# Kernel optimization log

Hardware: AMD Instinct MI355X
Metric: run time of the kernel (lower is better)

The kernel has to match this reference:

```python
import jax, jax.numpy as jnp
import numpy as np


def setup_inputs() -> dict:
    key = jax.random.key(0)
    k1, k2 = jax.random.split(key)
    B, T, S, D = 8, 1024, 1024, 2048
    support_sets = jax.random.normal(k1, (B, S, D), dtype=jnp.float32)
    X_hats = jax.random.normal(k2, (B, T, D), dtype=jnp.float32)
    return {"support_sets": support_sets, "X_hats": X_hats}


def reference(support_sets, X_hats):
    # Pairwise cosine similarity: out[b, t, s] = cos(X_hats[b, t], support_sets[b, s])
    # Matches torch.nn.functional.cosine_similarity with eps=1e-10:
    #   dot / max(||x|| * ||y||, eps)
    eps = 1e-10
    x_norm = jnp.linalg.norm(X_hats, axis=-1)          # [B, T]
    s_norm = jnp.linalg.norm(support_sets, axis=-1)    # [B, S]
    dots = jnp.einsum('btd,bsd->bts', X_hats, support_sets)  # [B, T, S]
    denom = jnp.maximum(x_norm[:, :, None] * s_norm[:, None, :], eps)
    return dots / denom
```

## Files before the change

kernel.cpp:

```cpp
#include <hip/hip_runtime.h>
#include <hip/hip_bf16.h>

typedef __attribute__((ext_vector_type(4))) float        f32x4;
typedef __attribute__((ext_vector_type(8))) short        s16x8;
typedef __attribute__((ext_vector_type(4))) unsigned int u32x4;
typedef __attribute__((ext_vector_type(2))) unsigned int u32x2;

#define Bb 8
#define Tt 1024
#define Ss 1024
#define Dd 2048
#define BM 128
#define BN 128
#define BK 64

__device__ __forceinline__ unsigned pack2_bf16(float f0, float f1) {
  unsigned u0 = __builtin_bit_cast(unsigned, f0) + 0x8000u;
  unsigned u1 = __builtin_bit_cast(unsigned, f1) + 0x8000u;
  return (u0 >> 16) | (u1 & 0xffff0000u);
}

__device__ __forceinline__ void gld_lds16(const void* g, void* l) {
  __builtin_amdgcn_global_load_lds(
      (__attribute__((address_space(1))) void*)(void*)(g),
      (__attribute__((address_space(3))) void*)l, 16, 0, 0);
}

__global__ __launch_bounds__(256, 8)
void convert_kernel(const float* __restrict__ src, unsigned* __restrict__ dst,
                    float* __restrict__ inv)
{
  __shared__ float red[4];
  const int row = blockIdx.x;
  const int t = threadIdx.x;
  const f32x4* s = (const f32x4*)(src + (size_t)row * Dd);
  const f32x4 a = s[t];
  const f32x4 b = s[256 + t];

  float sq = fmaf(a[0], a[0], fmaf(a[1], a[1], fmaf(a[2], a[2], a[3] * a[3])));
  sq = fmaf(b[0], b[0], fmaf(b[1], b[1], fmaf(b[2], b[2], fmaf(b[3], b[3], sq))));

  u32x2* d = (u32x2*)(dst + (size_t)row * (Dd / 2));
  d[t]       = (u32x2){pack2_bf16(a[0], a[1]), pack2_bf16(a[2], a[3])};
  d[256 + t] = (u32x2){pack2_bf16(b[0], b[1]), pack2_bf16(b[2], b[3])};

  #pragma unroll
  for (int m = 32; m; m >>= 1) sq += __shfl_xor(sq, m, 64);
  const int wave = t >> 6, lane = t & 63;
  if (lane == 0) red[wave] = sq;
  __syncthreads();
  if (t == 0) inv[row] = 1.0f / sqrtf(red[0] + red[1] + red[2] + red[3]);
}

__global__ __launch_bounds__(256, 2)
void gemm_kernel(const short* __restrict__ abf, const short* __restrict__ bbf,
                 const float* __restrict__ invA, const float* __restrict__ invB,
                 float* __restrict__ out)
{
  __shared__ short As[2][BM * BK];
  __shared__ short Bs[2][BN * BK];

  const int bid0 = blockIdx.x;
  const int bid  = ((bid0 & 7) << 6) | (bid0 >> 3);
  const int b    = bid >> 6;
  const int tile = bid & 63;
  const int tm   = tile >> 3;
  const int tn   = tile & 7;

  const int t = threadIdx.x, wave = t >> 6, lane = t & 63;

  const int srow = lane >> 3;
  const int cph  = lane & 7;
  const int r0   = wave * 32;

  const size_t aRow = (size_t)(b * Tt + tm * BM);
  const size_t bRow = (size_t)(b * Ss + tn * BN);
  const short *gA0, *gA1, *gA2, *gA3, *gB0, *gB1, *gB2, *gB3;
  {
    int r;
    r = r0 + 0 * 8 + srow; gA0 = abf + (aRow + r) * Dd + (cph ^ (r & 7)) * 8;
                           gB0 = bbf + (bRow + r) * Dd + (cph ^ (r & 7)) * 8;
    r = r0 + 1 * 8 + srow; gA1 = abf + (aRow + r) * Dd + (cph ^ (r & 7)) * 8;
                           gB1 = bbf + (bRow + r) * Dd + (cph ^ (r & 7)) * 8;
    r = r0 + 2 * 8 + srow; gA2 = abf + (aRow + r) * Dd + (cph ^ (r & 7)) * 8;
                           gB2 = bbf + (bRow + r) * Dd + (cph ^ (r & 7)) * 8;
    r = r0 + 3 * 8 + srow; gA3 = abf + (aRow + r) * Dd + (cph ^ (r & 7)) * 8;
                           gB3 = bbf + (bRow + r) * Dd + (cph ^ (r & 7)) * 8;
  }

  const int wm = (wave >> 1) << 6;
  const int wn = (wave & 1) << 6;
  const int lm = lane & 15;
  const int kq = lane >> 4;

  f32x4 acc[4][4];
  #pragma unroll
  for (int i = 0; i < 4; ++i)
    #pragma unroll
    for (int j = 0; j < 4; ++j)
      acc[i][j] = (f32x4)0.0f;

#define STAGE(bi) do {                                                   \
    gld_lds16(gA0, As[bi] + (r0 + 0)  * BK);                             \
    gld_lds16(gA1, As[bi] + (r0 + 8)  * BK);                             \
    gld_lds16(gA2, As[bi] + (r0 + 16) * BK);                             \
    gld_lds16(gA3, As[bi] + (r0 + 24) * BK);                             \
    gld_lds16(gB0, Bs[bi] + (r0 + 0)  * BK);                             \
    gld_lds16(gB1, Bs[bi] + (r0 + 8)  * BK);                             \
    gld_lds16(gB2, Bs[bi] + (r0 + 16) * BK);                             \
    gld_lds16(gB3, Bs[bi] + (r0 + 24) * BK);                             \
    gA0 += BK; gA1 += BK; gA2 += BK; gA3 += BK;                          \
    gB0 += BK; gB1 += BK; gB2 += BK; gB3 += BK;                          \
  } while (0)

#define COMPUTE(bi) do {                                                 \
    _Pragma("unroll")                                                    \
    for (int ks = 0; ks < 2; ++ks) {                                     \
      const int pchunk = ((ks * 4 + kq) ^ (lm & 7)) * 8;                 \
      s16x8 af[4], bfr[4];                                               \
      _Pragma("unroll")                                                  \
      for (int i = 0; i < 4; ++i) {                                      \
        af[i]  = *(const s16x8*)(As[bi] + (wm + i * 16 + lm) * BK + pchunk); \
        bfr[i] = *(const s16x8*)(Bs[bi] + (wn + i * 16 + lm) * BK + pchunk); \
      }                                                                  \
      _Pragma("unroll")                                                  \
      for (int mi = 0; mi < 4; ++mi)                                     \
        _Pragma("unroll")                                                \
        for (int ni = 0; ni < 4; ++ni)                                   \
          acc[mi][ni] = __builtin_amdgcn_mfma_f32_16x16x32_bf16(af[mi], bfr[ni], acc[mi][ni], 0, 0, 0); \
    }                                                                    \
  } while (0)

#define WAIT_BAR(n) do {                                                 \
    asm volatile("s_waitcnt vmcnt(" #n ")" ::: "memory");                \
    __builtin_amdgcn_s_barrier();                                        \
    __builtin_amdgcn_sched_barrier(0);                                   \
  } while (0)

  STAGE(0);
  STAGE(1);

  for (int i = 0; i < 15; ++i) {
    WAIT_BAR(8);
    COMPUTE(0);
    __builtin_amdgcn_sched_barrier(0);
    __builtin_amdgcn_s_barrier();
    STAGE(0);
    WAIT_BAR(8);
    COMPUTE(1);
    __builtin_amdgcn_sched_barrier(0);
    __builtin_amdgcn_s_barrier();
    STAGE(1);
  }

  WAIT_BAR(8);
  COMPUTE(0);
  WAIT_BAR(0);
  COMPUTE(1);
#undef STAGE
#undef COMPUTE
#undef WAIT_BAR

  const float* iA = invA + b * Tt + tm * BM;
  const float* iB = invB + b * Ss + tn * BN;
  float* outb = out + (size_t)(b * Tt + tm * BM) * Ss + tn * BN;
  const int m0 = wm + kq * 4;
  const int n0 = wn + lm;
  #pragma unroll
  for (int mi = 0; mi < 4; ++mi) {
    #pragma unroll
    for (int r = 0; r < 4; ++r) {
      const int mrow = m0 + mi * 16 + r;
      const float ia = iA[mrow];
      float* orow = outb + (size_t)mrow * Ss;
      #pragma unroll
      for (int ni = 0; ni < 4; ++ni) {
        const int ncol = n0 + ni * 16;
        orow[ncol] = acc[mi][ni][r] * (ia * iB[ncol]);
      }
    }
  }
}

#define LDKF 40
#define BKF 32
__global__ __launch_bounds__(256, 2)
void paircos_kernel(const float* __restrict__ sup, const float* __restrict__ xh,
                    float* __restrict__ out)
{
  __shared__ short As[BM * LDKF];
  __shared__ short Bs[BN * LDKF];
  __shared__ float invA[BM];
  __shared__ float invB[BN];

  const int bid = blockIdx.x;
  const int b = bid >> 6, tile = bid & 63, tm = tile >> 3, tn = tile & 7;
  const float* Abase = xh  + (size_t)(b * Tt + tm * BM) * Dd;
  const float* Bbase = sup + (size_t)(b * Ss + tn * BN) * Dd;
  const int t = threadIdx.x, row = t >> 1, kh = t & 1;
  const f32x4* agp = (const f32x4*)(Abase + (size_t)row * Dd + kh * 16);
  const f32x4* bgp = (const f32x4*)(Bbase + (size_t)row * Dd + kh * 16);
  u32x4* awr = (u32x4*)(As + row * LDKF + kh * 16);
  u32x4* bwr = (u32x4*)(Bs + row * LDKF + kh * 16);
  const int wave = t >> 6, lane = t & 63;
  const int wm = (wave >> 1) << 6, wn = (wave & 1) << 6;
  const int lm = lane & 15, kq = lane >> 4;

  f32x4 acc[4][4];
  #pragma unroll
  for (int i = 0; i < 4; ++i)
    #pragma unroll
    for (int j = 0; j < 4; ++j) acc[i][j] = (f32x4)0.0f;
  float sqa = 0.0f, sqb = 0.0f;
  f32x4 areg[4], breg[4];
  #pragma unroll
  for (int i = 0; i < 4; ++i) { areg[i] = agp[i]; breg[i] = bgp[i]; }

  for (int k0 = 0; k0 < Dd; k0 += BKF) {
    unsigned pa[8], pb[8];
    #pragma unroll
    for (int i = 0; i < 4; ++i) {
      sqa = fmaf(areg[i][0], areg[i][0], sqa); sqa = fmaf(areg[i][1], areg[i][1], sqa);
      sqa = fmaf(areg[i][2], areg[i][2], sqa); sqa = fmaf(areg[i][3], areg[i][3], sqa);
      pa[i*2+0] = pack2_bf16(areg[i][0], areg[i][1]); pa[i*2+1] = pack2_bf16(areg[i][2], areg[i][3]);
      sqb = fmaf(breg[i][0], breg[i][0], sqb); sqb = fmaf(breg[i][1], breg[i][1], sqb);
      sqb = fmaf(breg[i][2], breg[i][2], sqb); sqb = fmaf(breg[i][3], breg[i][3], sqb);
      pb[i*2+0] = pack2_bf16(breg[i][0], breg[i][1]); pb[i*2+1] = pack2_bf16(breg[i][2], breg[i][3]);
    }
    __syncthreads();
    awr[0] = (u32x4){pa[0],pa[1],pa[2],pa[3]}; awr[1] = (u32x4){pa[4],pa[5],pa[6],pa[7]};
    bwr[0] = (u32x4){pb[0],pb[1],pb[2],pb[3]}; bwr[1] = (u32x4){pb[4],pb[5],pb[6],pb[7]};
    __syncthreads();
    if (k0 + BKF < Dd) {
      const int off = (k0 + BKF) >> 2;
      #pragma unroll
      for (int i = 0; i < 4; ++i) { areg[i] = agp[off + i]; breg[i] = bgp[off + i]; }
    }
    s16x8 af[4], bfr[4];
    #pragma unroll
    for (int i = 0; i < 4; ++i) {
      af[i]  = *(const s16x8*)(As + (wm + i*16 + lm) * LDKF + kq * 8);
      bfr[i] = *(const s16x8*)(Bs + (wn + i*16 + lm) * LDKF + kq * 8);
    }
    #pragma unroll
    for (int mi = 0; mi < 4; ++mi)
      #pragma unroll
      for (int ni = 0; ni < 4; ++ni)
        acc[mi][ni] = __builtin_amdgcn_mfma_f32_16x16x32_bf16(af[mi], bfr[ni], acc[mi][ni], 0, 0, 0);
  }
  __syncthreads();
  ((float*)As)[t] = sqa; ((float*)Bs)[t] = sqb;
  __syncthreads();
  if (t < 128) {
    invA[t] = 1.0f / sqrtf(((float*)As)[2*t] + ((float*)As)[2*t+1]);
    invB[t] = 1.0f / sqrtf(((float*)Bs)[2*t] + ((float*)Bs)[2*t+1]);
  }
  __syncthreads();
  float* outb = out + (size_t)(b * Tt + tm * BM) * Ss + tn * BN;
  const int m0 = wm + kq * 4, n0 = wn + lm;
  #pragma unroll
  for (int mi = 0; mi < 4; ++mi) {
    #pragma unroll
    for (int r = 0; r < 4; ++r) {
      const int mrow = m0 + mi * 16 + r;
      const float ia = invA[mrow];
      float* orow = outb + (size_t)mrow * Ss;
      #pragma unroll
      for (int ni = 0; ni < 4; ++ni) {
        const int ncol = n0 + ni * 16;
        orow[ncol] = acc[mi][ni][r] * (ia * invB[ncol]);
      }
    }
  }
}

extern "C" void kernel_launch(void* const* d_in, const int* in_sizes, int n_in,
                              void* d_out, int out_size, void* d_ws, size_t ws_size,
                              hipStream_t stream) {
  const float* sup = (const float*)d_in[0];
  const float* xh  = (const float*)d_in[1];
  float* out = (float*)d_out;

  const size_t nElem = (size_t)Bb * Tt * Dd;
  const size_t bfBytes = nElem * sizeof(short);
  const size_t NEED = 2 * bfBytes + 2 * (size_t)Bb * Tt * sizeof(float);

  if (ws_size >= NEED) {
    unsigned* abf = (unsigned*)d_ws;
    unsigned* bbf = (unsigned*)((char*)d_ws + bfBytes);
    float* invA = (float*)((char*)d_ws + 2 * bfBytes);
    float* invB = invA + (size_t)Bb * Tt;
    convert_kernel<<<dim3(8192), dim3(256), 0, stream>>>(xh, abf, invA);
    convert_kernel<<<dim3(8192), dim3(256), 0, stream>>>(sup, bbf, invB);
    gemm_kernel<<<dim3(512), dim3(256), 0, stream>>>((const short*)abf, (const short*)bbf,
                                                     invA, invB, out);
  } else {
    paircos_kernel<<<dim3(512), dim3(256), 0, stream>>>(sup, xh, out);
  }
}
```

Before: 193.1 us.

## Enlarge GEMM tile to 256x128 with 8 waves, split phases with setprio

The GEMM block grows from 128x128 with 4 waves to 256x128 with 8 waves, halving the grid to 256 blocks and reusing each staged B tile across twice as many rows. The per-stage compute is split into two k-phases separated by barriers, and the MFMA sections are wrapped in s_setprio so waves interleave memory and matrix work. The aim is less global/LDS traffic per FLOP and better latency hiding. The cost is more LDS per block, extra barriers, and a grid of only 256 blocks, which may underfill the GPU's 256 CUs or leave a tail.

```diff
diff --git a/kernel.cpp b/kernel.cpp
--- a/kernel.cpp
+++ b/kernel.cpp
@@ -13,6 +13,8 @@
 #define BM 128
 #define BN 128
 #define BK 64
+#define BM2 256
+#define BN2 128
 
 __device__ __forceinline__ unsigned pack2_bf16(float f0, float f1) {
   unsigned u0 = __builtin_bit_cast(unsigned, f0) + 0x8000u;
@@ -52,40 +54,37 @@
   if (t == 0) inv[row] = 1.0f / sqrtf(red[0] + red[1] + red[2] + red[3]);
 }
 
-__global__ __launch_bounds__(256, 2)
+__global__ __launch_bounds__(512, 2)
 void gemm_kernel(const short* __restrict__ abf, const short* __restrict__ bbf,
                  const float* __restrict__ invA, const float* __restrict__ invB,
                  float* __restrict__ out)
 {
-  __shared__ short As[2][BM * BK];
-  __shared__ short Bs[2][BN * BK];
+  __shared__ short As[2][BM2 * BK];
+  __shared__ short Bs[2][BN2 * BK];
 
   const int bid0 = blockIdx.x;
-  const int bid  = ((bid0 & 7) << 6) | (bid0 >> 3);
-  const int b    = bid >> 6;
-  const int tile = bid & 63;
+  const int bid  = ((bid0 & 7) << 5) | (bid0 >> 3);
+  const int b    = bid >> 5;
+  const int tile = bid & 31;
   const int tm   = tile >> 3;
   const int tn   = tile & 7;
 
   const int t = threadIdx.x, wave = t >> 6, lane = t & 63;
-
   const int srow = lane >> 3;
   const int cph  = lane & 7;
-  const int r0   = wave * 32;
-
-  const size_t aRow = (size_t)(b * Tt + tm * BM);
-  const size_t bRow = (size_t)(b * Ss + tn * BN);
-  const short *gA0, *gA1, *gA2, *gA3, *gB0, *gB1, *gB2, *gB3;
+  const int lw8  = wave * 8;
+
+  const size_t aRow = (size_t)(b * Tt + tm * BM2);
+  const size_t bRow = (size_t)(b * Ss + tn * BN2);
+  const short *gA0, *gA1, *gA2, *gA3, *gB0, *gB1;
   {
     int r;
-    r = r0 + 0 * 8 + srow; gA0 = abf + (aRow + r) * Dd + (cph ^ (r & 7)) * 8;
-                           gB0 = bbf + (bRow + r) * Dd + (cph ^ (r & 7)) * 8;
-    r = r0 + 1 * 8 + srow; gA1 = abf + (aRow + r) * Dd + (cph ^ (r & 7)) * 8;
-                           gB1 = bbf + (bRow + r) * Dd + (cph ^ (r & 7)) * 8;
-    r = r0 + 2 * 8 + srow; gA2 = abf + (aRow + r) * Dd + (cph ^ (r & 7)) * 8;
-                           gB2 = bbf + (bRow + r) * Dd + (cph ^ (r & 7)) * 8;
-    r = r0 + 3 * 8 + srow; gA3 = abf + (aRow + r) * Dd + (cph ^ (r & 7)) * 8;
-                           gB3 = bbf + (bRow + r) * Dd + (cph ^ (r & 7)) * 8;
+    r = 0 * 64 + lw8 + srow; gA0 = abf + (aRow + r) * Dd + (cph ^ (r & 7)) * 8;
+                             gB0 = bbf + (bRow + r) * Dd + (cph ^ (r & 7)) * 8;
+    r = 1 * 64 + lw8 + srow; gA1 = abf + (aRow + r) * Dd + (cph ^ (r & 7)) * 8;
+                             gB1 = bbf + (bRow + r) * Dd + (cph ^ (r & 7)) * 8;
+    r = 2 * 64 + lw8 + srow; gA2 = abf + (aRow + r) * Dd + (cph ^ (r & 7)) * 8;
+    r = 3 * 64 + lw8 + srow; gA3 = abf + (aRow + r) * Dd + (cph ^ (r & 7)) * 8;
   }
 
   const int wm = (wave >> 1) << 6;
@@ -101,69 +100,75 @@
       acc[i][j] = (f32x4)0.0f;
 
 #define STAGE(bi) do {                                                   \
-    gld_lds16(gA0, As[bi] + (r0 + 0)  * BK);                             \
-    gld_lds16(gA1, As[bi] + (r0 + 8)  * BK);                             \
-    gld_lds16(gA2, As[bi] + (r0 + 16) * BK);                             \
-    gld_lds16(gA3, As[bi] + (r0 + 24) * BK);                             \
-    gld_lds16(gB0, Bs[bi] + (r0 + 0)  * BK);                             \
-    gld_lds16(gB1, Bs[bi] + (r0 + 8)  * BK);                             \
-    gld_lds16(gB2, Bs[bi] + (r0 + 16) * BK);                             \
-    gld_lds16(gB3, Bs[bi] + (r0 + 24) * BK);                             \
-    gA0 += BK; gA1 += BK; gA2 += BK; gA3 += BK;                          \
-    gB0 += BK; gB1 += BK; gB2 += BK; gB3 += BK;                          \
+    gld_lds16(gA0, As[bi] + (0 * 64 + lw8) * BK);                        \
+    gld_lds16(gA1, As[bi] + (1 * 64 + lw8) * BK);                        \
+    gld_lds16(gA2, As[bi] + (2 * 64 + lw8) * BK);                        \
+    gld_lds16(gA3, As[bi] + (3 * 64 + lw8) * BK);                        \
+    gld_lds16(gB0, Bs[bi] + (0 * 64 + lw8) * BK);                        \
+    gld_lds16(gB1, Bs[bi] + (1 * 64 + lw8) * BK);                        \
+    gA0 += BK; gA1 += BK; gA2 += BK; gA3 += BK; gB0 += BK; gB1 += BK;    \
   } while (0)
 
-#define COMPUTE(bi) do {                                                 \
+#define PHASE(bi, ks) do {                                               \
+    const int pchunk = ((ks * 4 + kq) ^ (lm & 7)) * 8;                   \
+    s16x8 af[4], bfr[4];                                                 \
     _Pragma("unroll")                                                    \
-    for (int ks = 0; ks < 2; ++ks) {                                     \
-      const int pchunk = ((ks * 4 + kq) ^ (lm & 7)) * 8;                 \
-      s16x8 af[4], bfr[4];                                               \
+    for (int i = 0; i < 4; ++i) {                                        \
+      af[i]  = *(const s16x8*)(As[bi] + (wm + i * 16 + lm) * BK + pchunk); \
+      bfr[i] = *(const s16x8*)(Bs[bi] + (wn + i * 16 + lm) * BK + pchunk); \
+    }                                                                    \
+    __builtin_amdgcn_s_setprio(1);                                       \
+    _Pragma("unroll")                                                    \
+    for (int mi = 0; mi < 4; ++mi)                                       \
       _Pragma("unroll")                                                  \
-      for (int i = 0; i < 4; ++i) {                                      \
-        af[i]  = *(const s16x8*)(As[bi] + (wm + i * 16 + lm) * BK + pchunk); \
-        bfr[i] = *(const s16x8*)(Bs[bi] + (wn + i * 16 + lm) * BK + pchunk); \
-      }                                                                  \
-      _Pragma("unroll")                                                  \
-      for (int mi = 0; mi < 4; ++mi)                                     \
-        _Pragma("unroll")                                                \
-        for (int ni = 0; ni < 4; ++ni)                                   \
-          acc[mi][ni] = __builtin_amdgcn_mfma_f32_16x16x32_bf16(af[mi], bfr[ni], acc[mi][ni], 0, 0, 0); \
-    }                                                                    \
+      for (int ni = 0; ni < 4; ++ni)                                     \
+        acc[mi][ni] = __builtin_amdgcn_mfma_f32_16x16x32_bf16(af[mi], bfr[ni], acc[mi][ni], 0, 0, 0); \
+    __builtin_amdgcn_s_setprio(0);                                       \
   } while (0)
 
+#define SB __builtin_amdgcn_sched_barrier(0)
 #define WAIT_BAR(n) do {                                                 \
     asm volatile("s_waitcnt vmcnt(" #n ")" ::: "memory");                \
     __builtin_amdgcn_s_barrier();                                        \
-    __builtin_amdgcn_sched_barrier(0);                                   \
+    SB;                                                                  \
   } while (0)
+#define MID_BAR do { SB; __builtin_amdgcn_s_barrier(); SB; } while (0)
 
   STAGE(0);
   STAGE(1);
 
   for (int i = 0; i < 15; ++i) {
-    WAIT_BAR(8);
-    COMPUTE(0);
-    __builtin_amdgcn_sched_barrier(0);
-    __builtin_amdgcn_s_barrier();
+    WAIT_BAR(6);
+    PHASE(0, 0);
+    MID_BAR;
+    PHASE(0, 1);
+    MID_BAR;
     STAGE(0);
-    WAIT_BAR(8);
-    COMPUTE(1);
-    __builtin_amdgcn_sched_barrier(0);
-    __builtin_amdgcn_s_barrier();
+    WAIT_BAR(6);
+    PHASE(1, 0);
+    MID_BAR;
+    PHASE(1, 1);
+    MID_BAR;
     STAGE(1);
   }
 
-  WAIT_BAR(8);
-  COMPUTE(0);
+  WAIT_BAR(6);
+  PHASE(0, 0);
+  MID_BAR;
+  PHASE(0, 1);
   WAIT_BAR(0);
-  COMPUTE(1);
+  PHASE(1, 0);
+  MID_BAR;
+  PHASE(1, 1);
 #undef STAGE
-#undef COMPUTE
+#undef PHASE
 #undef WAIT_BAR
-
-  const float* iA = invA + b * Tt + tm * BM;
-  const float* iB = invB + b * Ss + tn * BN;
-  float* outb = out + (size_t)(b * Tt + tm * BM) * Ss + tn * BN;
+#undef MID_BAR
+#undef SB
+
+  const float* iA = invA + b * Tt + tm * BM2;
+  const float* iB = invB + b * Ss + tn * BN2;
+  float* outb = out + (size_t)(b * Tt + tm * BM2) * Ss + tn * BN2;
   const int m0 = wm + kq * 4;
   const int n0 = wn + lm;
   #pragma unroll
@@ -292,7 +297,7 @@
     float* invB = invA + (size_t)Bb * Tt;
     convert_kernel<<<dim3(8192), dim3(256), 0, stream>>>(xh, abf, invA);
     convert_kernel<<<dim3(8192), dim3(256), 0, stream>>>(sup, bbf, invB);
-    gemm_kernel<<<dim3(512), dim3(256), 0, stream>>>((const short*)abf, (const short*)bbf,
+    gemm_kernel<<<dim3(256), dim3(512), 0, stream>>>((const short*)abf, (const short*)bbf,
                                                      invA, invB, out);
   } else {
     paircos_kernel<<<dim3(512), dim3(256), 0, stream>>>(sup, xh, out);
```

After: 198.0 us. 1.03x slower.
